# Performance work log

Hardware: AMD Instinct MI355X
Metric: run time of the kernel (lower is better)

Reference implementation:

```python
import jax, jax.numpy as jnp
import numpy as np

A = 9               # anchors per location (3 scales x 3 ratios)
STRIDE = 32         # backbone stride 16 * conv1 stride 2
PRE_NMS = 2000      # boxes kept before NMS
POST_NMS = 300      # rois kept after NMS
NMS_THRESH = 0.7
MIN_SIZE = 16.0
NEG = jnp.float32(-1e30)


def _generate_anchors(base_size=16, ratios=(0.5, 1.0, 2.0), scales=(8, 16, 32)):
    xc = yc = 0.5 * (base_size - 1)
    size = float(base_size * base_size)
    anchors = []
    for r in ratios:
        ws = np.round(np.sqrt(size / r))
        hs = np.round(ws * r)
        for s in scales:
            w, h = ws * s, hs * s
            anchors.append([xc - 0.5 * (w - 1), yc - 0.5 * (h - 1),
                            xc + 0.5 * (w - 1), yc + 0.5 * (h - 1)])
    return np.array(anchors, dtype=np.float32)  # [A,4]


def _conv(x, w, b, stride, pad):
    y = jax.lax.conv_general_dilated(
        x, w, (stride, stride), ((pad, pad), (pad, pad)),
        dimension_numbers=('NCHW', 'OIHW', 'NCHW'))
    return y + b[None, :, None, None]


def _iou_matrix(boxes):
    x1, y1, x2, y2 = boxes[:, 0], boxes[:, 1], boxes[:, 2], boxes[:, 3]
    area = (x2 - x1 + 1.0) * (y2 - y1 + 1.0)
    iw = jnp.maximum(0.0, jnp.minimum(x2[:, None], x2[None, :]) - jnp.maximum(x1[:, None], x1[None, :]) + 1.0)
    ih = jnp.maximum(0.0, jnp.minimum(y2[:, None], y2[None, :]) - jnp.maximum(y1[:, None], y1[None, :]) + 1.0)
    inter = iw * ih
    return inter / (area[:, None] + area[None, :] - inter)


def _nms_single(boxes, scores):
    # boxes [K,4] sorted by score desc; scores [K] (NEG = filtered out)
    K = boxes.shape[0]
    iou = _iou_matrix(boxes)
    prio = jnp.arange(K, 0, -1)

    def step(valid, _):
        any_valid = jnp.any(valid)
        pick = jnp.argmax(jnp.where(valid, prio, 0))
        new_valid = valid & (iou[pick] <= NMS_THRESH)
        return new_valid, (pick, any_valid)

    valid0 = scores > NEG * 0.5
    _, (picks, flags) = jax.lax.scan(step, valid0, None, length=POST_NMS)
    sel = boxes[picks] * flags[:, None].astype(boxes.dtype)
    return sel, jnp.sum(flags.astype(jnp.int32))


def _proposal(deltas, scores):
    B, _, H, W = deltas.shape
    im_h, im_w = float(H * STRIDE), float(W * STRIDE)
    anchors = jnp.asarray(_generate_anchors())  # [A,4]
    sx = (jnp.arange(W) * STRIDE).astype(jnp.float32)
    sy = (jnp.arange(H) * STRIDE).astype(jnp.float32)
    gx, gy = jnp.meshgrid(sx, sy)  # [H,W] each
    shift = jnp.stack([gx, gy, gx, gy], axis=-1)  # [H,W,4]
    anc = (shift[:, :, None, :] + anchors[None, None, :, :]).reshape(-1, 4)  # [H*W*A,4]

    d = deltas.reshape(B, A, 4, H, W).transpose(0, 3, 4, 1, 2).reshape(B, -1, 4)  # [B,N,4]
    s = scores[:, A:].transpose(0, 2, 3, 1).reshape(B, -1)  # fg scores [B,N]

    ws = anc[:, 2] - anc[:, 0] + 1.0
    hs = anc[:, 3] - anc[:, 1] + 1.0
    cx = anc[:, 0] + 0.5 * ws
    cy = anc[:, 1] + 0.5 * hs
    pcx = d[:, :, 0] * ws + cx
    pcy = d[:, :, 1] * hs + cy
    pw = jnp.exp(d[:, :, 2]) * ws
    ph = jnp.exp(d[:, :, 3]) * hs
    boxes = jnp.stack([pcx - 0.5 * pw, pcy - 0.5 * ph,
                       pcx + 0.5 * pw, pcy + 0.5 * ph], axis=-1)  # [B,N,4]
    lim = jnp.array([im_w - 1, im_h - 1, im_w - 1, im_h - 1], jnp.float32)
    boxes = jnp.minimum(jnp.maximum(boxes, 0.0), lim)

    bw = boxes[..., 2] - boxes[..., 0] + 1.0
    bh = boxes[..., 3] - boxes[..., 1] + 1.0
    s = jnp.where((bw >= MIN_SIZE) & (bh >= MIN_SIZE), s, NEG)

    top_s, idx = jax.lax.top_k(s, PRE_NMS)  # sorted desc
    top_b = jnp.take_along_axis(boxes, idx[:, :, None], axis=1)  # [B,PRE,4]

    sel, num = jax.vmap(_nms_single)(top_b, top_s)  # [B,POST,4], [B]
    bidx = jnp.broadcast_to(jnp.arange(B, dtype=sel.dtype)[:, None, None], (B, POST_NMS, 1))
    rois = jnp.concatenate([bidx, sel], axis=-1)  # [B,POST,5]
    return rois, num


def setup_inputs() -> dict:
    key = jax.random.key(0)
    k = jax.random.split(key, 4)
    x = jax.random.normal(k[0], (4, 512, 96, 160), jnp.float32)
    w1 = jax.random.normal(k[1], (512, 512, 3, 3), jnp.float32) * 0.02
    b1 = jnp.zeros((512,), jnp.float32)
    w_bbox = jax.random.normal(k[2], (36, 512, 1, 1), jnp.float32) * 0.02
    b_bbox = jnp.zeros((36,), jnp.float32)
    w_cls = jax.random.normal(k[3], (18, 512, 3, 3), jnp.float32) * 0.02
    b_cls = jnp.zeros((18,), jnp.float32)
    return dict(x=x, w1=w1, b1=b1, w_bbox=w_bbox, b_bbox=b_bbox, w_cls=w_cls, b_cls=b_cls)


def reference(x, w1, b1, w_bbox, b_bbox, w_cls, b_cls):
    feat = _conv(x, w1, b1, 2, 1)           # [B,512,H/2,W/2]
    deltas = _conv(feat, w_bbox, b_bbox, 1, 0)  # [B,36,h,w]
    cls = _conv(feat, w_cls, b_cls, 1, 1)       # [B,18,h,w]
    return _proposal(deltas, cls)
```

## Files before the change

### kernel.cpp

```cpp
#include <hip/hip_runtime.h>
#include <stdint.h>

typedef unsigned long long u64;
typedef unsigned int u32;

__constant__ float c_aw[9] = {184.f,368.f,736.f,128.f,256.f,512.f, 88.f,176.f,352.f};
__constant__ float c_ah[9] = { 96.f,192.f,384.f,128.f,256.f,512.f,176.f,352.f,704.f};

__global__ __launch_bounds__(256) void transpose_k(const float* __restrict__ w1,
                                                   float* __restrict__ wt2) {
  int e = blockIdx.x * 256 + threadIdx.x;
  int m = e & 7;
  int t = e >> 3;
  int k = t % 9;
  int r = t / 9;
  int ci = r & 511;
  int g = r >> 9;
  wt2[e] = w1[(size_t)(g * 8 + m) * 4608 + ci * 9 + k];
}

__global__ __launch_bounds__(256, 3) void conv1_k(const float* __restrict__ x,
                                                  const float* __restrict__ wt2,
                                                  const float* __restrict__ b1,
                                                  float* __restrict__ feat) {
  __shared__ float xs[8 * 9 * 164];
  const int tid = threadIdx.x;
  const int lane = tid & 63;
  const int wv = __builtin_amdgcn_readfirstlane(tid >> 6);
  const int owg = lane & 15;
  const int ohl = lane >> 4;
  const int n = blockIdx.z;
  const int gg = blockIdx.x * 4 + wv;
  const int oh0 = blockIdx.y * 4;
  const int ih_base = 2 * oh0 - 1;

  int soff[6], loff[6];
  float okf[6];
  bool act[6];
#pragma unroll
  for (int it = 0; it < 6; ++it) {
    int e2 = tid + 256 * it;
    act[it] = (e2 < 1449);
    int e = act[it] ? e2 : 0;
    int ih = e / 161;
    int c = e - ih * 161;
    int gih = ih_base + ih;
    int giw = c - 1;
    bool ok = act[it] && ((unsigned)gih < 96u) && ((unsigned)giw < 160u);
    int cg = min(max(gih, 0), 95);
    int cw = min(max(giw, 0), 159);
    soff[it] = cg * 160 + cw;
    loff[it] = ih * 164 + c;
    okf[it] = ok ? 1.f : 0.f;
  }

  float acc[8][5];
#pragma unroll
  for (int m = 0; m < 8; ++m)
#pragma unroll
    for (int j = 0; j < 5; ++j) acc[m][j] = 0.f;

  const float* xb = x + (size_t)n * 512 * 96 * 160;
  const float* wgb = wt2 + (size_t)gg * 512 * 72;

  float r[6][8];
#pragma unroll
  for (int it = 0; it < 6; ++it)
#pragma unroll
    for (int ci = 0; ci < 8; ++ci)
      r[it][ci] = xb[(size_t)ci * 15360 + soff[it]];

  for (int c0 = 0; c0 < 512; c0 += 8) {
    __syncthreads();
#pragma unroll
    for (int it = 0; it < 6; ++it) {
      if (act[it]) {
        const float m_ = okf[it];
#pragma unroll
        for (int ci = 0; ci < 8; ++ci)
          xs[loff[it] + ci * 1476] = m_ * r[it][ci];
      }
    }
    __syncthreads();
    if (c0 + 8 < 512) {
      const float* xn = xb + (size_t)(c0 + 8) * 15360;
#pragma unroll
      for (int it = 0; it < 6; ++it)
#pragma unroll
        for (int ci = 0; ci < 8; ++ci)
          r[it][ci] = xn[(size_t)ci * 15360 + soff[it]];
    }

    for (int ci = 0; ci < 8; ++ci) {
      const float* wp = wgb + (size_t)(c0 + ci) * 72;
      const float* xrow = &xs[(ci * 9 + 2 * ohl) * 164 + owg * 10];
#pragma unroll
      for (int kh = 0; kh < 3; ++kh) {
        float xv[12];
        const float* xr = xrow + kh * 164;
#pragma unroll
        for (int t2 = 0; t2 < 6; ++t2) {
          float2 t = *(const float2*)(xr + 2 * t2);
          xv[2 * t2] = t.x; xv[2 * t2 + 1] = t.y;
        }
#pragma unroll
        for (int kw = 0; kw < 3; ++kw) {
          const float* wk = wp + (kh * 3 + kw) * 8;
#pragma unroll
          for (int j = 0; j < 5; ++j) {
            const float xj = xv[kw + 2 * j];
            acc[0][j] += wk[0] * xj; acc[1][j] += wk[1] * xj;
            acc[2][j] += wk[2] * xj; acc[3][j] += wk[3] * xj;
            acc[4][j] += wk[4] * xj; acc[5][j] += wk[5] * xj;
            acc[6][j] += wk[6] * xj; acc[7][j] += wk[7] * xj;
          }
        }
      }
    }
  }
  const int oh = oh0 + ohl;
  const int owb = owg * 5;
#pragma unroll
  for (int m = 0; m < 8; ++m) {
    const int co = gg * 8 + m;
    const float bv = b1[co];
    float* op = &feat[(((size_t)n * 512 + co) * 48 + oh) * 80 + owb];
#pragma unroll
    for (int j = 0; j < 5; ++j) op[j] = acc[m][j] + bv;
  }
}

__global__ __launch_bounds__(256) void heads_k(const float* __restrict__ feat,
                                               const float* __restrict__ wb,
                                               const float* __restrict__ bb,
                                               const float* __restrict__ wcg,
                                               const float* __restrict__ bc,
                                               float* __restrict__ deltas,
                                               float* __restrict__ s) {
  __shared__ float smem[5328];
  const int tid = threadIdx.x;

  if (blockIdx.x < 120) {
    float* fs  = smem;
    float* wsb = smem + 2048;
    const int blk = blockIdx.x;
    const int b = blk / 30;
    const int pos0 = (blk % 30) * 128;
    const int pl = tid >> 1, cg = tid & 1;
    const int cbase = cg * 18;
    float acc[18];
#pragma unroll
    for (int j = 0; j < 18; ++j) acc[j] = 0.f;
    const float* fb = feat + (size_t)b * 512 * 3840;

    for (int c0 = 0; c0 < 512; c0 += 16) {
      for (int e = tid; e < 16 * 128; e += 256)
        fs[e] = fb[(size_t)(c0 + (e >> 7)) * 3840 + pos0 + (e & 127)];
      for (int e = tid; e < 16 * 36; e += 256) {
        int ci = e / 36, c = e - ci * 36;
        wsb[e] = wb[(size_t)c * 512 + c0 + ci];
      }
      __syncthreads();
      for (int ci = 0; ci < 16; ++ci) {
        float xv = fs[ci * 128 + pl];
#pragma unroll
        for (int j = 0; j < 18; ++j) acc[j] += xv * wsb[ci * 36 + cbase + j];
      }
      __syncthreads();
    }
    size_t o = ((size_t)b * 3840 + pos0 + pl) * 36 + cbase;
#pragma unroll
    for (int j = 0; j < 18; ++j) deltas[o + j] = acc[j] + bb[cbase + j];
  } else {
    float (*fs)[3][84] = (float(*)[3][84])smem;
    float (*wc)[9][9]  = (float(*)[9][9])(smem + 4032);
    const int bid2 = blockIdx.x - 120;
    const int oh = bid2 % 48;
    const int b = bid2 / 48;
    const int pos = tid % 80;
    const int cg = tid / 80;
    float acc[3] = {0.f, 0.f, 0.f};
    const float* fb = feat + (size_t)b * 512 * 3840;

    for (int c0 = 0; c0 < 512; c0 += 16) {
      for (int e = tid; e < 16 * 246; e += 256) {
        int ci = e / 246;
        int r = e - ci * 246;
        int ihl = r / 82;
        int iw = r - ihl * 82 - 1;
        int gih = oh - 1 + ihl;
        float v = 0.f;
        if ((unsigned)gih < 48u && (unsigned)iw < 80u)
          v = fb[(size_t)(c0 + ci) * 3840 + gih * 80 + iw];
        fs[ci][ihl][iw + 1] = v;
      }
      for (int e = tid; e < 16 * 81; e += 256) {
        int ci = e / 81;
        int r = e - ci * 81;
        int co = r / 9;
        int k = r - co * 9;
        wc[ci][co][k] = wcg[((size_t)(9 + co) * 512 + c0 + ci) * 9 + k];
      }
      __syncthreads();
      if (cg < 3) {
        const int cb = cg * 3;
        for (int ci = 0; ci < 16; ++ci) {
#pragma unroll
          for (int kh = 0; kh < 3; ++kh) {
#pragma unroll
            for (int kw = 0; kw < 3; ++kw) {
              float xv = fs[ci][kh][pos + kw];
              acc[0] += xv * wc[ci][cb + 0][kh * 3 + kw];
              acc[1] += xv * wc[ci][cb + 1][kh * 3 + kw];
              acc[2] += xv * wc[ci][cb + 2][kh * 3 + kw];
            }
          }
        }
      }
      __syncthreads();
    }
    if (cg < 3) {
      const int cb = cg * 3;
      size_t o = (size_t)b * 34560 + ((size_t)oh * 80 + pos) * 9 + cb;
#pragma unroll
      for (int j = 0; j < 3; ++j) s[o + j] = acc[j] + bc[9 + cb + j];
    }
  }
}

__global__ __launch_bounds__(256) void decode_k(const float* __restrict__ deltas,
                                                const float* __restrict__ s,
                                                float* __restrict__ boxes,
                                                u64* __restrict__ keys) {
  const int g = blockIdx.x * 256 + threadIdx.x;
  const int b = g / 34560;
  const int i = g - b * 34560;
  const int pos = i / 9;
  const int a = i - pos * 9;
  const int h = pos / 80;
  const int w = pos - h * 80;
  const float gx = (float)(w * 32);
  const float gy = (float)(h * 32);
  const float aw = c_aw[a], ah = c_ah[a];
  const float x1a = 7.5f - 0.5f * (aw - 1.f);
  const float y1a = 7.5f - 0.5f * (ah - 1.f);
  const float ws_ = aw, hs_ = ah;
  const float cx = (gx + x1a) + 0.5f * ws_;
  const float cy = (gy + y1a) + 0.5f * hs_;

  const float* dp = &deltas[((size_t)b * 3840 + pos) * 36 + a * 4];
  const float d0 = dp[0], d1 = dp[1], d2 = dp[2], d3 = dp[3];
  const float pcx = __fadd_rn(__fmul_rn(d0, ws_), cx);
  const float pcy = __fadd_rn(__fmul_rn(d1, hs_), cy);
  const float pw = __fmul_rn(expf(d2), ws_);
  const float ph = __fmul_rn(expf(d3), hs_);
  float bx1 = __fsub_rn(pcx, __fmul_rn(0.5f, pw));
  float by1 = __fsub_rn(pcy, __fmul_rn(0.5f, ph));
  float bx2 = __fadd_rn(pcx, __fmul_rn(0.5f, pw));
  float by2 = __fadd_rn(pcy, __fmul_rn(0.5f, ph));
  bx1 = fminf(fmaxf(bx1, 0.f), 2559.f);
  by1 = fminf(fmaxf(by1, 0.f), 1535.f);
  bx2 = fminf(fmaxf(bx2, 0.f), 2559.f);
  by2 = fminf(fmaxf(by2, 0.f), 1535.f);
  const float bw = __fadd_rn(__fsub_rn(bx2, bx1), 1.f);
  const float bh = __fadd_rn(__fsub_rn(by2, by1), 1.f);
  float sc = s[g];
  if (!(bw >= 16.f && bh >= 16.f)) sc = -1e30f;

  float4 bo;
  bo.x = bx1; bo.y = by1; bo.z = bx2; bo.w = by2;
  *(float4*)&boxes[(size_t)g * 4] = bo;

  u32 sb = __float_as_uint(sc);
  u32 ou = (sb & 0x80000000u) ? ~sb : (sb | 0x80000000u);
  keys[g] = ((u64)ou << 32) | (u32)(~(u32)i);
}

__global__ __launch_bounds__(1024) void selcomp_k(const u64* __restrict__ keys,
                                                  u64* __restrict__ sel) {
  __shared__ u32 h[2048];
  __shared__ int s_bin;
  __shared__ u32 s_above;
  __shared__ int sc;
  const int b = blockIdx.x;
  const int tid = threadIdx.x;
  const u64* kb = keys + (size_t)b * 34560;
  u64 prefix = 0, pmask = 0;
  int rank = 2000;

#pragma unroll 1
  for (int pass = 0; pass < 6; ++pass) {
    int shift = 53 - 11 * pass;
    if (shift < 0) shift = 0;
    h[tid] = 0; h[tid + 1024] = 0;
    __syncthreads();
    for (int i = tid; i < 34560; i += 1024) {
      u64 k = kb[i];
      if ((k & pmask) == prefix)
        atomicAdd(&h[(u32)((k >> shift) & 2047ull)], 1u);
    }
    __syncthreads();
    for (int off = 1; off < 2048; off <<= 1) {
      u32 t0, t1;
      { int i = tid;        t0 = h[i] + ((i + off < 2048) ? h[i + off] : 0u); }
      { int i = tid + 1024; t1 = h[i] + ((i + off < 2048) ? h[i + off] : 0u); }
      __syncthreads();
      h[tid] = t0; h[tid + 1024] = t1;
      __syncthreads();
    }
#pragma unroll
    for (int q = 0; q < 2; ++q) {
      int i = tid + 1024 * q;
      u32 Si = h[i];
      u32 Sn = (i < 2047) ? h[i + 1] : 0u;
      if ((int)Si >= rank && (int)Sn < rank) { s_bin = i; s_above = Sn; }
    }
    __syncthreads();
    rank -= (int)s_above;
    prefix |= ((u64)(u32)s_bin) << shift;
    pmask |= (2047ull << shift);
    __syncthreads();
  }
  if (tid == 0) sc = 0;
  __syncthreads();
  for (int i = tid; i < 34560; i += 1024) {
    u64 k = kb[i];
    if (k >= prefix) {
      int p = atomicAdd(&sc, 1);
      sel[(size_t)b * 2048 + p] = k;
    }
  }
}

__global__ __launch_bounds__(1024) void nms2_k(const u64* __restrict__ sel,
                                               const float* __restrict__ boxes,
                                               float* __restrict__ out) {
  __shared__ u64 K[2048];
  __shared__ float bx1[2000], by1[2000], bx2[2000], by2[2000], ar[2000];
  __shared__ unsigned char val[2000];
  __shared__ int s_pick, s_cur, s_cnt;
  const int b = blockIdx.x;
  const int tid = threadIdx.x;

  for (int i = tid; i < 2048; i += 1024)
    K[i] = (i < 2000) ? sel[(size_t)b * 2048 + i] : 0ull;
  __syncthreads();
  for (int k2 = 2; k2 <= 2048; k2 <<= 1) {
    for (int j = k2 >> 1; j > 0; j >>= 1) {
      for (int i = tid; i < 2048; i += 1024) {
        int l = i ^ j;
        if (l > i) {
          u64 a = K[i], c = K[l];
          bool up = ((i & k2) == 0);
          if (up ? (a < c) : (a > c)) { K[i] = c; K[l] = a; }
        }
      }
      __syncthreads();
    }
  }
  for (int i = tid; i < 2000; i += 1024) {
    u64 key = K[i];
    u32 ou = (u32)(key >> 32);
    int idx = (int)(~(u32)key);
    u32 sb = (ou & 0x80000000u) ? (ou & 0x7FFFFFFFu) : ~ou;
    float sc = __uint_as_float(sb);
    const float4 bo = *(const float4*)&boxes[((size_t)b * 34560 + idx) * 4];
    bx1[i] = bo.x; by1[i] = bo.y; bx2[i] = bo.z; by2[i] = bo.w;
    ar[i] = __fmul_rn(__fadd_rn(__fsub_rn(bo.z, bo.x), 1.f),
                      __fadd_rn(__fsub_rn(bo.w, bo.y), 1.f));
    val[i] = (sc > -5e29f) ? 1 : 0;
  }
  if (tid == 0) { s_cur = 0; s_cnt = 0; }
  __syncthreads();

  for (int t = 0; t < 300; ++t) {
    if (tid == 0) {
      int c = s_cur;
      while (c < 2000 && !val[c]) ++c;
      if (c < 2000) { s_pick = c; s_cur = c + 1; s_cnt = t + 1; }
      else s_pick = -1;
    }
    __syncthreads();
    const int p = s_pick;
    if (p < 0) break;
    const float px1 = bx1[p], py1 = by1[p], px2 = bx2[p], py2 = by2[p], pa = ar[p];
    if (tid == 0) {
      float* row = out + ((size_t)b * 300 + t) * 5;
      row[0] = (float)b; row[1] = px1; row[2] = py1; row[3] = px2; row[4] = py2;
    }
    for (int jj = p + 1 + tid; jj < 2000; jj += 1024) {
      if (val[jj]) {
        float iw = __fadd_rn(__fsub_rn(fminf(px2, bx2[jj]), fmaxf(px1, bx1[jj])), 1.f);
        iw = fmaxf(0.f, iw);
        float ih = __fadd_rn(__fsub_rn(fminf(py2, by2[jj]), fmaxf(py1, by1[jj])), 1.f);
        ih = fmaxf(0.f, ih);
        float inter = __fmul_rn(iw, ih);
        float denom = __fsub_rn(__fadd_rn(pa, ar[jj]), inter);
        float iou = __fdiv_rn(inter, denom);
        if (iou > 0.7f) val[jj] = 0;
      }
    }
    __syncthreads();
  }

  __syncthreads();
  const int cnt = s_cnt;
  for (int t = cnt + tid; t < 300; t += 1024) {
    float* row = out + ((size_t)b * 300 + t) * 5;
    row[0] = (float)b; row[1] = 0.f; row[2] = 0.f; row[3] = 0.f; row[4] = 0.f;
  }
  if (tid == 0) out[6000 + b] = (float)cnt;
}

extern "C" void kernel_launch(void* const* d_in, const int* in_sizes, int n_in,
                              void* d_out, int out_size, void* d_ws, size_t ws_size,
                              hipStream_t stream) {
  const float* x  = (const float*)d_in[0];
  const float* w1 = (const float*)d_in[1];
  const float* b1 = (const float*)d_in[2];
  const float* wb = (const float*)d_in[3];
  const float* bb = (const float*)d_in[4];
  const float* wc = (const float*)d_in[5];
  const float* bc = (const float*)d_in[6];
  float* out = (float*)d_out;
  char* ws = (char*)d_ws;

  float* feat   = (float*)(ws + 0);
  float* wt2    = (float*)(ws + 31457280);
  float* deltas = (float*)(ws + 40894464);
  float* s      = (float*)(ws + 43106304);
  float* boxes  = (float*)(ws + 43659264);
  u64*   keys   = (u64*)  (ws + 45871104);
  u64*   sel    = (u64*)  (ws + 46977088);

  hipLaunchKernelGGL(transpose_k, dim3(9216), dim3(256), 0, stream, w1, wt2);
  hipLaunchKernelGGL(conv1_k, dim3(16, 12, 4), dim3(256), 0, stream, x, wt2, b1, feat);
  hipLaunchKernelGGL(heads_k, dim3(312), dim3(256), 0, stream, feat, wb, bb, wc, bc, deltas, s);
  hipLaunchKernelGGL(decode_k, dim3(540), dim3(256), 0, stream, deltas, s, boxes, keys);
  hipLaunchKernelGGL(selcomp_k, dim3(4), dim3(1024), 0, stream, keys, sel);
  hipLaunchKernelGGL(nms2_k, dim3(4), dim3(1024), 0, stream, sel, boxes, out);
}
```

Before: 1.599 ms.

## Replace six-pass radix select with single 14-bit histogram and parallel NMS pick

The top-k selection now builds one 16384-bin histogram on the top 14 key bits, finds the threshold bin with a wave-shuffle suffix scan, and ranks the boundary-bin candidates by pairwise comparison. This replaces the six histogram and scan passes. NMS no longer has one thread serially scan for the next valid box; surviving boxes do an atomicMin into a double-buffered next-pick slot while suppression runs. The risks are the quadratic ranking cost if the boundary bin is large, and extra shared-memory atomics in the NMS loop.

Result: slower. 3.365 ms (+110.4%).

```diff
diff --git a/kernel.cpp b/kernel.cpp
--- a/kernel.cpp
+++ b/kernel.cpp
@@ -47,9 +47,7 @@
     int gih = ih_base + ih;
     int giw = c - 1;
     bool ok = act[it] && ((unsigned)gih < 96u) && ((unsigned)giw < 160u);
-    int cg = min(max(gih, 0), 95);
-    int cw = min(max(giw, 0), 159);
-    soff[it] = cg * 160 + cw;
+    soff[it] = min(max(gih, 0), 95) * 160 + min(max(giw, 0), 159);
     loff[it] = ih * 164 + c;
     okf[it] = ok ? 1.f : 0.f;
   }
@@ -100,8 +98,8 @@
         const float* xr = xrow + kh * 164;
 #pragma unroll
         for (int t2 = 0; t2 < 6; ++t2) {
-          float2 t = *(const float2*)(xr + 2 * t2);
-          xv[2 * t2] = t.x; xv[2 * t2 + 1] = t.y;
+          float2 tt = *(const float2*)(xr + 2 * t2);
+          xv[2 * t2] = tt.x; xv[2 * t2 + 1] = tt.y;
         }
 #pragma unroll
         for (int kw = 0; kw < 3; ++kw) {
@@ -278,57 +276,83 @@
 
 __global__ __launch_bounds__(1024) void selcomp_k(const u64* __restrict__ keys,
                                                   u64* __restrict__ sel) {
-  __shared__ u32 h[2048];
-  __shared__ int s_bin;
-  __shared__ u32 s_above;
-  __shared__ int sc;
+  __shared__ u32 h[16384];
+  __shared__ u64 cand[6144];
+  __shared__ u32 wsum[16], wsuf[16];
+  __shared__ int s_bin, s_above, s_main, s_nc;
   const int b = blockIdx.x;
   const int tid = threadIdx.x;
+  const int lane = tid & 63;
+  const int wv = tid >> 6;
   const u64* kb = keys + (size_t)b * 34560;
-  u64 prefix = 0, pmask = 0;
-  int rank = 2000;
-
-#pragma unroll 1
-  for (int pass = 0; pass < 6; ++pass) {
-    int shift = 53 - 11 * pass;
-    if (shift < 0) shift = 0;
-    h[tid] = 0; h[tid + 1024] = 0;
-    __syncthreads();
-    for (int i = tid; i < 34560; i += 1024) {
-      u64 k = kb[i];
-      if ((k & pmask) == prefix)
-        atomicAdd(&h[(u32)((k >> shift) & 2047ull)], 1u);
-    }
-    __syncthreads();
-    for (int off = 1; off < 2048; off <<= 1) {
-      u32 t0, t1;
-      { int i = tid;        t0 = h[i] + ((i + off < 2048) ? h[i + off] : 0u); }
-      { int i = tid + 1024; t1 = h[i] + ((i + off < 2048) ? h[i + off] : 0u); }
-      __syncthreads();
-      h[tid] = t0; h[tid + 1024] = t1;
-      __syncthreads();
-    }
-#pragma unroll
-    for (int q = 0; q < 2; ++q) {
-      int i = tid + 1024 * q;
-      u32 Si = h[i];
-      u32 Sn = (i < 2047) ? h[i + 1] : 0u;
-      if ((int)Si >= rank && (int)Sn < rank) { s_bin = i; s_above = Sn; }
-    }
-    __syncthreads();
-    rank -= (int)s_above;
-    prefix |= ((u64)(u32)s_bin) << shift;
-    pmask |= (2047ull << shift);
-    __syncthreads();
-  }
-  if (tid == 0) sc = 0;
-  __syncthreads();
+
+#pragma unroll
+  for (int q = 0; q < 16; ++q) h[tid + 1024 * q] = 0;
+  __syncthreads();
+  for (int i = tid; i < 34560; i += 1024)
+    atomicAdd(&h[(u32)(kb[i] >> 50)], 1u);
+  __syncthreads();
+
+  const int i0 = tid * 16;
+  u32 myb[16];
+  u32 tsum = 0;
+#pragma unroll
+  for (int q = 0; q < 16; ++q) { myb[q] = h[i0 + q]; tsum += myb[q]; }
+  u32 sfx = tsum;
+#pragma unroll
+  for (int off = 1; off < 64; off <<= 1) {
+    u32 o = __shfl_down(sfx, off, 64);
+    if (lane + off < 64) sfx += o;
+  }
+  if (lane == 0) wsum[wv] = sfx;
+  __syncthreads();
+  if (tid < 16) {
+    u32 v = wsum[tid];
+#pragma unroll
+    for (int off = 1; off < 16; off <<= 1) {
+      u32 o = __shfl_down(v, off, 64);
+      if (tid + off < 16) v += o;
+    }
+    wsuf[tid] = v;
+  }
+  __syncthreads();
+  const u32 wave_base = (wv < 15) ? wsuf[wv + 1] : 0u;
+  u32 accu = wave_base + (sfx - tsum);
+#pragma unroll
+  for (int q = 15; q >= 0; --q) { accu += myb[q]; h[i0 + q] = accu; }
+  __syncthreads();
+
+#pragma unroll
+  for (int q = 0; q < 16; ++q) {
+    int bn = i0 + q;
+    u32 Si = h[bn];
+    u32 Sn = (bn < 16383) ? h[bn + 1] : 0u;
+    if ((int)Si >= 2000 && (int)Sn < 2000) { s_bin = bn; s_above = (int)Sn; }
+  }
+  if (tid == 0) { s_main = 0; s_nc = 0; }
+  __syncthreads();
+  const u32 B = (u32)s_bin;
+  const int above = s_above;
+  const int need = 2000 - above;
+
   for (int i = tid; i < 34560; i += 1024) {
     u64 k = kb[i];
-    if (k >= prefix) {
-      int p = atomicAdd(&sc, 1);
+    u32 t14 = (u32)(k >> 50);
+    if (t14 > B) {
+      int p = atomicAdd(&s_main, 1);
       sel[(size_t)b * 2048 + p] = k;
-    }
+    } else if (t14 == B) {
+      int p = atomicAdd(&s_nc, 1);
+      if (p < 6144) cand[p] = k;
+    }
+  }
+  __syncthreads();
+  const int nc = min(s_nc, 6144);
+  for (int c = tid; c < nc; c += 1024) {
+    u64 kc = cand[c];
+    int rnk = 0;
+    for (int j = 0; j < nc; ++j) rnk += (cand[j] > kc) ? 1 : 0;
+    if (rnk < need) sel[(size_t)b * 2048 + above + rnk] = kc;
   }
 }
 
@@ -338,7 +362,8 @@
   __shared__ u64 K[2048];
   __shared__ float bx1[2000], by1[2000], bx2[2000], by2[2000], ar[2000];
   __shared__ unsigned char val[2000];
-  __shared__ int s_pick, s_cur, s_cnt;
+  __shared__ int nxt[2];
+  __shared__ int s_cnt;
   const int b = blockIdx.x;
   const int tid = threadIdx.x;
 
@@ -370,21 +395,21 @@
                       __fadd_rn(__fsub_rn(bo.w, bo.y), 1.f));
     val[i] = (sc > -5e29f) ? 1 : 0;
   }
-  if (tid == 0) { s_cur = 0; s_cnt = 0; }
+  if (tid == 0) { nxt[0] = 2000; nxt[1] = 2000; s_cnt = 0; }
+  __syncthreads();
+  for (int i = tid; i < 2000; i += 1024)
+    if (val[i]) atomicMin(&nxt[0], i);
   __syncthreads();
 
   for (int t = 0; t < 300; ++t) {
-    if (tid == 0) {
-      int c = s_cur;
-      while (c < 2000 && !val[c]) ++c;
-      if (c < 2000) { s_pick = c; s_cur = c + 1; s_cnt = t + 1; }
-      else s_pick = -1;
-    }
+    const int c = t & 1;
+    const int p = nxt[c];
+    if (p >= 2000) break;
     __syncthreads();
-    const int p = s_pick;
-    if (p < 0) break;
     const float px1 = bx1[p], py1 = by1[p], px2 = bx2[p], py2 = by2[p], pa = ar[p];
     if (tid == 0) {
+      nxt[c] = 2000;
+      s_cnt = t + 1;
       float* row = out + ((size_t)b * 300 + t) * 5;
       row[0] = (float)b; row[1] = px1; row[2] = py1; row[3] = px2; row[4] = py2;
     }
@@ -398,6 +423,7 @@
         float denom = __fsub_rn(__fadd_rn(pa, ar[jj]), inter);
         float iou = __fdiv_rn(inter, denom);
         if (iou > 0.7f) val[jj] = 0;
+        else atomicMin(&nxt[c ^ 1], jj);
       }
     }
     __syncthreads();
```
